# Kernel tuning notes

Hardware: AMD Instinct MI355X
Metric: run time of the kernel (lower is better)

## Reference

```python
import jax, jax.numpy as jnp
import numpy as np

N_USERS = 100000
N_ITEMS = 50000
DIM = 64
N_EDGES = 4_000_000
NUM_LAYERS = 3


def setup_inputs() -> dict:
    key = jax.random.key(0)
    k1, k2, k3 = jax.random.split(key, 3)
    # xavier_uniform-like scale for embeddings
    scale = float(np.sqrt(6.0 / (N_USERS + DIM)))
    user_emb = jax.random.uniform(k1, (N_USERS, DIM), jnp.float32, -scale, scale)
    scale_i = float(np.sqrt(6.0 / (N_ITEMS + DIM)))
    item_emb = jax.random.uniform(k2, (N_ITEMS, DIM), jnp.float32, -scale_i, scale_i)
    edge_index = jax.random.randint(k3, (2, N_EDGES), 0, N_USERS + N_ITEMS, dtype=jnp.int64)
    return {"user_emb": user_emb, "item_emb": item_emb, "edge_index": edge_index}


def reference(user_emb, item_emb, edge_index):
    """LightGCN_W.encode_window: K rounds of symmetric-normalized SpMM, then layer mean."""
    n_users = user_emb.shape[0]
    n_nodes = n_users + item_emb.shape[0]
    row, col = edge_index[0], edge_index[1]  # messages flow row (source) -> col (target)

    # gcn_norm with add_self_loops=False (PyG LGConv default)
    ones = jnp.ones(row.shape[0], dtype=user_emb.dtype)
    deg = jax.ops.segment_sum(ones, col, num_segments=n_nodes)
    dinv = jnp.where(deg > 0, jax.lax.rsqrt(jnp.maximum(deg, 1e-12)), 0.0)
    norm = (dinv[row] * dinv[col])[:, None]  # [E, 1]

    x = jnp.concatenate([user_emb, item_emb], axis=0)  # [N, D]
    acc = x
    for _ in range(NUM_LAYERS):
        x = jax.ops.segment_sum(norm * x[row], col, num_segments=n_nodes)
        acc = acc + x
    out = acc / (NUM_LAYERS + 1)
    return out[:n_users], out[n_users:]
```

## Files before the change

kernel.cpp:

```cpp
#include <hip/hip_runtime.h>
#include <hip/hip_fp16.h>

#define DIM 64
#define BSH 8
#define BMASK 255u
#define NBMAX 1024
#define BINC 16384


__global__ void zero_ints(int* __restrict__ p, int n) {
    int i = blockIdx.x * blockDim.x + threadIdx.x;
    if (i < n) p[i] = 0;
}

__global__ __launch_bounds__(1024) void bucket_count_kernel(const int* __restrict__ edge, int E,
                                                            int* __restrict__ bcnt, int NB) {
    __shared__ int lcnt[NBMAX];
    for (int i = threadIdx.x; i < NB; i += 1024) lcnt[i] = 0;
    __syncthreads();
    int stride = gridDim.x * 1024;
    for (int i = blockIdx.x * 1024 + threadIdx.x; i < E; i += stride)
        atomicAdd(&lcnt[edge[E + i] >> BSH], 1);
    __syncthreads();
    for (int i = threadIdx.x; i < NB; i += 1024) {
        int v = lcnt[i];
        if (v) atomicAdd(&bcnt[i], v);
    }
}

__global__ __launch_bounds__(1024) void scan_kernel(const int* __restrict__ cnt,
                                                    int* __restrict__ offsets,
                                                    int* __restrict__ cursor,
                                                    int n) {
    __shared__ int lds[1024];
    const int T = 1024, K = 4, CHUNK = T * K;
    int carry = 0;
    for (int base = 0; base < n; base += CHUNK) {
        int v[K];
        int idx0 = base + (int)threadIdx.x * K;
#pragma unroll
        for (int k = 0; k < K; ++k) {
            int i = idx0 + k;
            v[k] = (i < n) ? cnt[i] : 0;
        }
        int tsum = v[0] + v[1] + v[2] + v[3];
        lds[threadIdx.x] = tsum;
        __syncthreads();
        int incl = tsum;
        for (int off = 1; off < T; off <<= 1) {
            int t = (threadIdx.x >= (unsigned)off) ? lds[threadIdx.x - off] : 0;
            __syncthreads();
            incl += t;
            lds[threadIdx.x] = incl;
            __syncthreads();
        }
        int total = lds[T - 1];
        int run = carry + (incl - tsum);
#pragma unroll
        for (int k = 0; k < K; ++k) {
            int i = idx0 + k;
            if (i < n) { offsets[i] = run; cursor[i] = run; }
            run += v[k];
        }
        carry += total;
        __syncthreads();
    }
    if (threadIdx.x == 0) offsets[n] = carry;
}

__global__ __launch_bounds__(1024) void bin_kernel(const int* __restrict__ edge, int E,
                                                   int* __restrict__ bcur,
                                                   unsigned* __restrict__ bin, int NB) {
    __shared__ unsigned stage[BINC];
    __shared__ int lcnt[NBMAX];
    __shared__ int lsc[NBMAX];
    __shared__ int lcur[NBMAX];
    __shared__ int gb[NBMAX];
    const int tid = (int)threadIdx.x;
    const int beg = (int)blockIdx.x * BINC;
    const int n = min(BINC, E - beg);

    lcnt[tid] = 0;
    __syncthreads();
    for (int i = tid; i < n; i += 1024)
        atomicAdd(&lcnt[edge[E + beg + i] >> BSH], 1);
    __syncthreads();
    lsc[tid] = lcnt[tid];
    __syncthreads();
    for (int off = 1; off < 1024; off <<= 1) {
        int t = (tid >= off) ? lsc[tid - off] : 0;
        __syncthreads();
        lsc[tid] += t;
        __syncthreads();
    }
    {
        int cb = lcnt[tid];
        lcur[tid] = lsc[tid] - cb;
        if (tid < NB) gb[tid] = cb ? atomicAdd(&bcur[tid], cb) : 0;
    }
    __syncthreads();
    for (int i = tid; i < n; i += 1024) {
        int r = edge[beg + i];
        int c = edge[E + beg + i];
        int b = c >> BSH;
        int slot = atomicAdd(&lcur[b], 1);
        stage[slot] = ((unsigned)r << BSH) | ((unsigned)c & BMASK);
    }
    __syncthreads();
    const int wid = tid >> 6, lane = tid & 63;
    for (int b = wid; b < NB; b += 16) {
        int cb = lcnt[b];
        if (!cb) continue;
        int lb = lsc[b] - cb;
        int g = gb[b];
        for (int l = lane; l < cb; l += 64)
            bin[g + l] = stage[lb + l];
    }
}

__global__ __launch_bounds__(256) void csr_kernel(const unsigned* __restrict__ bin,
                                                  const int* __restrict__ boff,
                                                  int* __restrict__ offsets,
                                                  float* __restrict__ dinv,
                                                  int* __restrict__ row_sorted,
                                                  int nN) {
    __shared__ int lcnt[256];
    __shared__ int lsc[256];
    __shared__ int lcur[256];
    const int tid = (int)threadIdx.x;
    const int b = (int)blockIdx.x;
    const int beg = boff[b], end = boff[b + 1];
    lcnt[tid] = 0;
    __syncthreads();
    for (int i = beg + tid; i < end; i += 256)
        atomicAdd(&lcnt[bin[i] & BMASK], 1);
    __syncthreads();
    lsc[tid] = lcnt[tid];
    __syncthreads();
    for (int off = 1; off < 256; off <<= 1) {
        int t = (tid >= off) ? lsc[tid - off] : 0;
        __syncthreads();
        lsc[tid] += t;
        __syncthreads();
    }
    int cb = lcnt[tid];
    int lb = lsc[tid] - cb;
    lcur[tid] = lb;
    int node = (b << BSH) + tid;
    if (node < nN) {
        offsets[node] = beg + lb;
        dinv[node] = cb ? rsqrtf((float)cb) : 0.0f;
        if (node == nN - 1) offsets[nN] = beg + lsc[tid];
    }
    __syncthreads();
    for (int i = beg + tid; i < end; i += 256) {
        unsigned e = bin[i];
        int c = (int)(e & BMASK);
        int p = atomicAdd(&lcur[c], 1);
        row_sorted[beg + p] = (int)(e >> BSH);
    }
}

__global__ void init_kernel(const float* __restrict__ user,
                            const float* __restrict__ item,
                            const float* __restrict__ dinv,
                            float* __restrict__ out,
                            __half* __restrict__ y,
                            int nU, int total) {
    int i = blockIdx.x * blockDim.x + threadIdx.x;
    if (i < total) {
        int node = i >> 6;
        float v = (node < nU) ? user[i] : item[i - nU * DIM];
        out[i] = 0.25f * v;
        y[i] = __float2half(dinv[node] * v);
    }
}

template<bool LAST>
__global__ __launch_bounds__(256) void layer_kernel(const int* __restrict__ offsets,
                                                    const int* __restrict__ row_sorted,
                                                    const float* __restrict__ dinv,
                                                    const __half* __restrict__ y_in,
                                                    __half* __restrict__ y_out,
                                                    float* __restrict__ out,
                                                    int nN) {
    int wave = (int)((blockIdx.x * blockDim.x + threadIdx.x) >> 6);
    int lane = (int)(threadIdx.x & 63);
    if (wave >= nN) return;
    const int beg = offsets[wave];
    const int end = offsets[wave + 1];
    const int g = lane >> 3;
    const int q = lane & 7;
    const float4* yv = (const float4*)y_in;
    float a0 = 0, a1 = 0, a2 = 0, a3 = 0, a4 = 0, a5 = 0, a6 = 0, a7 = 0;
    const int last = end - 1;
    for (int base = beg; base < end; base += 16) {
        int e0 = base + g;
        int e1 = e0 + 8;
        int i0 = (e0 <= last) ? e0 : last;
        int i1 = (e1 <= last) ? e1 : last;
        float m0 = (e0 <= last) ? 1.0f : 0.0f;
        float m1 = (e1 <= last) ? 1.0f : 0.0f;
        int r0 = row_sorted[i0];
        int r1 = row_sorted[i1];
        float4 v0 = yv[(size_t)r0 * 8 + q];
        float4 v1 = yv[(size_t)r1 * 8 + q];
        const __half2* h0 = (const __half2*)&v0;
        const __half2* h1 = (const __half2*)&v1;
        float2 t;
        t = __half22float2(h0[0]); a0 = fmaf(m0, t.x, a0); a1 = fmaf(m0, t.y, a1);
        t = __half22float2(h0[1]); a2 = fmaf(m0, t.x, a2); a3 = fmaf(m0, t.y, a3);
        t = __half22float2(h0[2]); a4 = fmaf(m0, t.x, a4); a5 = fmaf(m0, t.y, a5);
        t = __half22float2(h0[3]); a6 = fmaf(m0, t.x, a6); a7 = fmaf(m0, t.y, a7);
        t = __half22float2(h1[0]); a0 = fmaf(m1, t.x, a0); a1 = fmaf(m1, t.y, a1);
        t = __half22float2(h1[1]); a2 = fmaf(m1, t.x, a2); a3 = fmaf(m1, t.y, a3);
        t = __half22float2(h1[2]); a4 = fmaf(m1, t.x, a4); a5 = fmaf(m1, t.y, a5);
        t = __half22float2(h1[3]); a6 = fmaf(m1, t.x, a6); a7 = fmaf(m1, t.y, a7);
    }
#pragma unroll
    for (int ofs = 8; ofs <= 32; ofs <<= 1) {
        a0 += __shfl_xor(a0, ofs);
        a1 += __shfl_xor(a1, ofs);
        a2 += __shfl_xor(a2, ofs);
        a3 += __shfl_xor(a3, ofs);
        a4 += __shfl_xor(a4, ofs);
        a5 += __shfl_xor(a5, ofs);
        a6 += __shfl_xor(a6, ofs);
        a7 += __shfl_xor(a7, ofs);
    }
    float dc = dinv[wave];
    if (g == 0) {
        float x0 = dc * a0, x1 = dc * a1, x2 = dc * a2, x3 = dc * a3;
        float x4 = dc * a4, x5 = dc * a5, x6 = dc * a6, x7 = dc * a7;
        float4* o4 = (float4*)(out + (size_t)wave * DIM + q * 8);
        float4 c0 = o4[0], c1 = o4[1];
        c0.x += 0.25f * x0; c0.y += 0.25f * x1; c0.z += 0.25f * x2; c0.w += 0.25f * x3;
        c1.x += 0.25f * x4; c1.y += 0.25f * x5; c1.z += 0.25f * x6; c1.w += 0.25f * x7;
        o4[0] = c0; o4[1] = c1;
        if (!LAST) {
            float4 pack;
            __half2* p = (__half2*)&pack;
            p[0] = __floats2half2_rn(dc * x0, dc * x1);
            p[1] = __floats2half2_rn(dc * x2, dc * x3);
            p[2] = __floats2half2_rn(dc * x4, dc * x5);
            p[3] = __floats2half2_rn(dc * x6, dc * x7);
            ((float4*)y_out)[(size_t)wave * 8 + q] = pack;
        }
    }
}


extern "C" void kernel_launch(void* const* d_in, const int* in_sizes, int n_in,
                              void* d_out, int out_size, void* d_ws, size_t ws_size,
                              hipStream_t stream) {
    const float* user = (const float*)d_in[0];
    const float* item = (const float*)d_in[1];
    const int*   edge = (const int*)d_in[2];

    const int nU = in_sizes[0] / DIM;
    const int nI = in_sizes[1] / DIM;
    const int nN = nU + nI;
    const int E  = in_sizes[2] / 2;
    const int total = nN * DIM;
    const int NB = (nN + 255) / 256;

    float* out = (float*)d_out;

    char* ws = (char*)d_ws;
    size_t off = 0;
    auto take = [&](size_t bytes) -> char* {
        char* p = ws + off;
        off = (off + bytes + 255) & ~(size_t)255;
        return p;
    };
    int*      bcnt       = (int*)     take((size_t)NB * 4);
    int*      boff       = (int*)     take((size_t)(NB + 1) * 4);
    int*      bcur       = (int*)     take((size_t)NB * 4);
    unsigned* bin        = (unsigned*)take((size_t)E * 4);
    int*      offsets    = (int*)     take((size_t)(nN + 1) * 4);
    float*    dinv       = (float*)   take((size_t)nN * 4);
    int*      row_sorted = (int*)     take((size_t)E * 4);
    __half*   y0         = (__half*)  take((size_t)total * 2);
    __half*   y1         = (__half*)  take((size_t)total * 2);
    (void)ws_size; (void)n_in; (void)out_size;

    const int B = 256;
    dim3 blk(B);

    zero_ints<<<dim3((NB + B - 1) / B), blk, 0, stream>>>(bcnt, NB);
    bucket_count_kernel<<<dim3(256), dim3(1024), 0, stream>>>(edge, E, bcnt, NB);
    scan_kernel<<<dim3(1), dim3(1024), 0, stream>>>(bcnt, boff, bcur, NB);
    bin_kernel<<<dim3((E + BINC - 1) / BINC), dim3(1024), 0, stream>>>(edge, E, bcur, bin, NB);
    csr_kernel<<<dim3(NB), blk, 0, stream>>>(bin, boff, offsets, dinv, row_sorted, nN);
    init_kernel<<<dim3((total + B - 1) / B), blk, 0, stream>>>(user, item, dinv, out, y0, nU, total);

    dim3 lgrid((nN + 3) / 4);
    layer_kernel<false><<<lgrid, blk, 0, stream>>>(offsets, row_sorted, dinv, y0, y1, out, nN);
    layer_kernel<false><<<lgrid, blk, 0, stream>>>(offsets, row_sorted, dinv, y1, y0, out, nN);
    layer_kernel<true ><<<lgrid, blk, 0, stream>>>(offsets, row_sorted, dinv, y0, nullptr, out, nN);
}
```

Before: 337.5 us.

## Fuse init into CSR build and defer output accumulation to a final pass

The separate init kernel is removed: the CSR kernel now writes the scaled fp16 input embeddings itself, reusing its shared degree values. Layer kernels no longer read and write the fp32 output each layer. They store only the fp16 propagated state (scaled by dinv squared). A new final kernel combines the original embeddings with the three layer states, multiplying by sqrt(deg), to form the mean. This saves three fp32 read-modify-write passes over the output at the cost of an extra fp16 buffer and a recovery step through sqrt(deg), which adds some fp16 rounding error. Workspace buffers are aliased so the CSR bin buffer doubles as a layer buffer.

```diff
diff --git a/kernel.cpp b/kernel.cpp
--- a/kernel.cpp
+++ b/kernel.cpp
@@ -120,13 +120,19 @@
 
 __global__ __launch_bounds__(256) void csr_kernel(const unsigned* __restrict__ bin,
                                                   const int* __restrict__ boff,
+                                                  const float* __restrict__ user,
+                                                  const float* __restrict__ item,
+                                                  int nU,
                                                   int* __restrict__ offsets,
                                                   float* __restrict__ dinv,
+                                                  float* __restrict__ rdinv,
                                                   int* __restrict__ row_sorted,
+                                                  __half* __restrict__ y0,
                                                   int nN) {
     __shared__ int lcnt[256];
     __shared__ int lsc[256];
     __shared__ int lcur[256];
+    __shared__ float sdinv[256];
     const int tid = (int)threadIdx.x;
     const int b = (int)blockIdx.x;
     const int beg = boff[b], end = boff[b + 1];
@@ -146,10 +152,13 @@
     int cb = lcnt[tid];
     int lb = lsc[tid] - cb;
     lcur[tid] = lb;
+    float dv = cb ? rsqrtf((float)cb) : 0.0f;
+    sdinv[tid] = dv;
     int node = (b << BSH) + tid;
     if (node < nN) {
         offsets[node] = beg + lb;
-        dinv[node] = cb ? rsqrtf((float)cb) : 0.0f;
+        dinv[node] = dv;
+        rdinv[node] = cb ? sqrtf((float)cb) : 0.0f;
         if (node == nN - 1) offsets[nN] = beg + lsc[tid];
     }
     __syncthreads();
@@ -159,30 +168,35 @@
         int p = atomicAdd(&lcur[c], 1);
         row_sorted[beg + p] = (int)(e >> BSH);
     }
-}
-
-__global__ void init_kernel(const float* __restrict__ user,
-                            const float* __restrict__ item,
-                            const float* __restrict__ dinv,
-                            float* __restrict__ out,
-                            __half* __restrict__ y,
-                            int nU, int total) {
-    int i = blockIdx.x * blockDim.x + threadIdx.x;
-    if (i < total) {
-        int node = i >> 6;
-        float v = (node < nU) ? user[i] : item[i - nU * DIM];
-        out[i] = 0.25f * v;
-        y[i] = __float2half(dinv[node] * v);
-    }
-}
-
-template<bool LAST>
+    const int baseNode = b << BSH;
+#pragma unroll
+    for (int it = 0; it < 8; ++it) {
+        int idx = it * 256 + tid;
+        int ln = idx >> 3;
+        int node2 = baseNode + ln;
+        if (node2 < nN) {
+            int qc = idx & 7;
+            const float* src = (node2 < nU) ? user + (size_t)node2 * DIM
+                                            : item + (size_t)(node2 - nU) * DIM;
+            float4 e0 = ((const float4*)src)[qc * 2];
+            float4 e1 = ((const float4*)src)[qc * 2 + 1];
+            float dvn = sdinv[ln];
+            float4 pack;
+            __half2* p = (__half2*)&pack;
+            p[0] = __floats2half2_rn(dvn * e0.x, dvn * e0.y);
+            p[1] = __floats2half2_rn(dvn * e0.z, dvn * e0.w);
+            p[2] = __floats2half2_rn(dvn * e1.x, dvn * e1.y);
+            p[3] = __floats2half2_rn(dvn * e1.z, dvn * e1.w);
+            ((float4*)y0)[(size_t)baseNode * 8 + idx] = pack;
+        }
+    }
+}
+
 __global__ __launch_bounds__(256) void layer_kernel(const int* __restrict__ offsets,
                                                     const int* __restrict__ row_sorted,
                                                     const float* __restrict__ dinv,
                                                     const __half* __restrict__ y_in,
                                                     __half* __restrict__ y_out,
-                                                    float* __restrict__ out,
                                                     int nN) {
     int wave = (int)((blockIdx.x * blockDim.x + threadIdx.x) >> 6);
     int lane = (int)(threadIdx.x & 63);
@@ -228,25 +242,62 @@
         a6 += __shfl_xor(a6, ofs);
         a7 += __shfl_xor(a7, ofs);
     }
-    float dc = dinv[wave];
     if (g == 0) {
-        float x0 = dc * a0, x1 = dc * a1, x2 = dc * a2, x3 = dc * a3;
-        float x4 = dc * a4, x5 = dc * a5, x6 = dc * a6, x7 = dc * a7;
-        float4* o4 = (float4*)(out + (size_t)wave * DIM + q * 8);
-        float4 c0 = o4[0], c1 = o4[1];
-        c0.x += 0.25f * x0; c0.y += 0.25f * x1; c0.z += 0.25f * x2; c0.w += 0.25f * x3;
-        c1.x += 0.25f * x4; c1.y += 0.25f * x5; c1.z += 0.25f * x6; c1.w += 0.25f * x7;
-        o4[0] = c0; o4[1] = c1;
-        if (!LAST) {
-            float4 pack;
-            __half2* p = (__half2*)&pack;
-            p[0] = __floats2half2_rn(dc * x0, dc * x1);
-            p[1] = __floats2half2_rn(dc * x2, dc * x3);
-            p[2] = __floats2half2_rn(dc * x4, dc * x5);
-            p[3] = __floats2half2_rn(dc * x6, dc * x7);
-            ((float4*)y_out)[(size_t)wave * 8 + q] = pack;
-        }
-    }
+        float dc = dinv[wave];
+        float s = dc * dc;
+        float4 pack;
+        __half2* p = (__half2*)&pack;
+        p[0] = __floats2half2_rn(s * a0, s * a1);
+        p[1] = __floats2half2_rn(s * a2, s * a3);
+        p[2] = __floats2half2_rn(s * a4, s * a5);
+        p[3] = __floats2half2_rn(s * a6, s * a7);
+        ((float4*)y_out)[(size_t)wave * 8 + q] = pack;
+    }
+}
+
+__global__ __launch_bounds__(256) void final_kernel(const float* __restrict__ user,
+                                                    const float* __restrict__ item,
+                                                    const float* __restrict__ rdinv,
+                                                    const __half* __restrict__ y1,
+                                                    const __half* __restrict__ y2,
+                                                    const __half* __restrict__ y3,
+                                                    float* __restrict__ out,
+                                                    int nU, int nN) {
+    int c = blockIdx.x * blockDim.x + threadIdx.x;
+    if (c >= nN * 8) return;
+    int node = c >> 3;
+    int qc = c & 7;
+    float rd = 0.25f * rdinv[node];
+    float4 h1 = ((const float4*)y1)[c];
+    float4 h2 = ((const float4*)y2)[c];
+    float4 h3 = ((const float4*)y3)[c];
+    const float* src = (node < nU) ? user + (size_t)node * DIM
+                                   : item + (size_t)(node - nU) * DIM;
+    float4 e0 = ((const float4*)src)[qc * 2];
+    float4 e1 = ((const float4*)src)[qc * 2 + 1];
+    const __half2* p1 = (const __half2*)&h1;
+    const __half2* p2 = (const __half2*)&h2;
+    const __half2* p3 = (const __half2*)&h3;
+    float r[8];
+#pragma unroll
+    for (int j = 0; j < 4; ++j) {
+        float2 u1 = __half22float2(p1[j]);
+        float2 u2 = __half22float2(p2[j]);
+        float2 u3 = __half22float2(p3[j]);
+        r[2 * j]     = u1.x + u2.x + u3.x;
+        r[2 * j + 1] = u1.y + u2.y + u3.y;
+    }
+    float4 o0, o1;
+    o0.x = 0.25f * e0.x + rd * r[0];
+    o0.y = 0.25f * e0.y + rd * r[1];
+    o0.z = 0.25f * e0.z + rd * r[2];
+    o0.w = 0.25f * e0.w + rd * r[3];
+    o1.x = 0.25f * e1.x + rd * r[4];
+    o1.y = 0.25f * e1.y + rd * r[5];
+    o1.z = 0.25f * e1.z + rd * r[6];
+    o1.w = 0.25f * e1.w + rd * r[7];
+    ((float4*)out)[(size_t)c * 2]     = o0;
+    ((float4*)out)[(size_t)c * 2 + 1] = o1;
 }
 
 
@@ -273,15 +324,23 @@
         off = (off + bytes + 255) & ~(size_t)255;
         return p;
     };
-    int*      bcnt       = (int*)     take((size_t)NB * 4);
-    int*      boff       = (int*)     take((size_t)(NB + 1) * 4);
-    int*      bcur       = (int*)     take((size_t)NB * 4);
-    unsigned* bin        = (unsigned*)take((size_t)E * 4);
-    int*      offsets    = (int*)     take((size_t)(nN + 1) * 4);
-    float*    dinv       = (float*)   take((size_t)nN * 4);
-    int*      row_sorted = (int*)     take((size_t)E * 4);
-    __half*   y0         = (__half*)  take((size_t)total * 2);
-    __half*   y1         = (__half*)  take((size_t)total * 2);
+    const size_t ybytes = (size_t)total * 2;
+    const size_t binbytes = (size_t)E * 4;
+    int*      bcnt       = (int*)  take((size_t)NB * 4);
+    int*      boff       = (int*)  take((size_t)(NB + 1) * 4);
+    int*      bcur       = (int*)  take((size_t)NB * 4);
+    int*      offsets    = (int*)  take((size_t)(nN + 1) * 4);
+    float*    dinv       = (float*)take((size_t)nN * 4);
+    float*    rdinv      = (float*)take((size_t)nN * 4);
+    int*      row_sorted = (int*)  take((size_t)E * 4);
+    char*     regionA    = take(binbytes > ybytes ? binbytes : ybytes);
+    char*     regionB    = take(ybytes);
+    char*     regionC    = take(ybytes);
+    unsigned* bin = (unsigned*)regionA;
+    __half*   y1  = (__half*)regionA;
+    __half*   y0  = (__half*)regionB;
+    __half*   y3  = (__half*)regionB;
+    __half*   y2  = (__half*)regionC;
     (void)ws_size; (void)n_in; (void)out_size;
 
     const int B = 256;
@@ -291,11 +350,14 @@
     bucket_count_kernel<<<dim3(256), dim3(1024), 0, stream>>>(edge, E, bcnt, NB);
     scan_kernel<<<dim3(1), dim3(1024), 0, stream>>>(bcnt, boff, bcur, NB);
     bin_kernel<<<dim3((E + BINC - 1) / BINC), dim3(1024), 0, stream>>>(edge, E, bcur, bin, NB);
-    csr_kernel<<<dim3(NB), blk, 0, stream>>>(bin, boff, offsets, dinv, row_sorted, nN);
-    init_kernel<<<dim3((total + B - 1) / B), blk, 0, stream>>>(user, item, dinv, out, y0, nU, total);
+    csr_kernel<<<dim3(NB), blk, 0, stream>>>(bin, boff, user, item, nU,
+                                             offsets, dinv, rdinv, row_sorted, y0, nN);
 
     dim3 lgrid((nN + 3) / 4);
-    layer_kernel<false><<<lgrid, blk, 0, stream>>>(offsets, row_sorted, dinv, y0, y1, out, nN);
-    layer_kernel<false><<<lgrid, blk, 0, stream>>>(offsets, row_sorted, dinv, y1, y0, out, nN);
-    layer_kernel<true ><<<lgrid, blk, 0, stream>>>(offsets, row_sorted, dinv, y0, nullptr, out, nN);
-}
+    layer_kernel<<<lgrid, blk, 0, stream>>>(offsets, row_sorted, dinv, y0, y1, nN);
+    layer_kernel<<<lgrid, blk, 0, stream>>>(offsets, row_sorted, dinv, y1, y2, nN);
+    layer_kernel<<<lgrid, blk, 0, stream>>>(offsets, row_sorted, dinv, y2, y3, nN);
+
+    final_kernel<<<dim3((nN * 8 + B - 1) / B), blk, 0, stream>>>(user, item, rdinv,
+                                                                 y1, y2, y3, out, nU, nN);
+}
```

New measurement: 319.2 us. 5.4% less time.
